# Optimization experiments

Hardware: AMD Instinct MI355X
Metric: run time of the kernel (lower is better)

The kernel has to match this reference:

```python
import jax, jax.numpy as jnp
import numpy as np

D_MODEL = 512
N_HEADS = 4  # d_model >= 8 -> 4 heads
HEAD_DIM = D_MODEL // N_HEADS
D_FF = 4 * D_MODEL


def setup_inputs() -> dict:
    key = jax.random.key(0)
    ks = jax.random.split(key, 8)
    B, T = 4, 2048
    s = 0.02
    return {
        "x": jax.random.normal(ks[0], (B, T, D_MODEL), dtype=jnp.float32),
        "ln1_g": jnp.ones((D_MODEL,), jnp.float32),
        "ln1_b": jnp.zeros((D_MODEL,), jnp.float32),
        "w_qkv": jax.random.normal(ks[1], (D_MODEL, 3 * D_MODEL), jnp.float32) * s,
        "w_proj": jax.random.normal(ks[2], (D_MODEL, D_MODEL), jnp.float32) * s,
        "ln2_g": jnp.ones((D_MODEL,), jnp.float32),
        "ln2_b": jnp.zeros((D_MODEL,), jnp.float32),
        "w_ff1": jax.random.normal(ks[3], (D_MODEL, D_FF), jnp.float32) * s,
        "w_ff2": jax.random.normal(ks[4], (D_FF, D_MODEL), jnp.float32) * s,
    }


def _layernorm(x, g, b, eps=1e-5):
    mu = jnp.mean(x, axis=-1, keepdims=True)
    var = jnp.var(x, axis=-1, keepdims=True)
    return (x - mu) * jax.lax.rsqrt(var + eps) * g + b


def _attention(x, w_qkv, w_proj):
    B, T, C = x.shape
    qkv = x @ w_qkv  # [B,T,3C]
    q, k, v = jnp.split(qkv, 3, axis=-1)
    # [B,H,T,Dh]
    q = q.reshape(B, T, N_HEADS, HEAD_DIM).transpose(0, 2, 1, 3)
    k = k.reshape(B, T, N_HEADS, HEAD_DIM).transpose(0, 2, 1, 3)
    v = v.reshape(B, T, N_HEADS, HEAD_DIM).transpose(0, 2, 1, 3)
    scale = 1.0 / jnp.sqrt(jnp.asarray(HEAD_DIM, x.dtype))
    scores = jnp.einsum("bhqd,bhkd->bhqk", q, k) * scale
    causal = jnp.tril(jnp.ones((T, T), bool))
    scores = jnp.where(causal, scores, -jnp.inf)
    attn = jax.nn.softmax(scores, axis=-1)
    out = jnp.einsum("bhqk,bhkd->bhqd", attn, v)
    out = out.transpose(0, 2, 1, 3).reshape(B, T, C)
    return out @ w_proj


def reference(x, ln1_g, ln1_b, w_qkv, w_proj, ln2_g, ln2_b, w_ff1, w_ff2):
    x = x + _attention(_layernorm(x, ln1_g, ln1_b), w_qkv, w_proj)
    h = _layernorm(x, ln2_g, ln2_b)
    h = jax.nn.gelu(h @ w_ff1, approximate=False) @ w_ff2
    return x + h
```

## Files before the change

### kernel.cpp

```cpp
#include <hip/hip_runtime.h>
#include <cstdint>

typedef unsigned short u16;
typedef __attribute__((ext_vector_type(8))) short short8;
typedef __attribute__((ext_vector_type(4))) float floatx4;

#define BT    8192
#define TSEQ  2048
#define NBAT  4
#define CMOD  512
#define NH    4
#define HD    128
#define DFF   2048
#define CQKV  1536

__device__ __forceinline__ u16 f2bf(float f) {
  union { float f; uint32_t u; } v; v.f = f;
  uint32_t r = v.u + 0x7FFFu + ((v.u >> 16) & 1u);
  return (u16)(r >> 16);
}
__device__ __forceinline__ float bf2f(u16 u) {
  union { uint32_t u; float f; } v; v.u = ((uint32_t)u) << 16; return v.f;
}
__device__ __forceinline__ float exp2a(float x) {
  float r; asm("v_exp_f32 %0, %1" : "=v"(r) : "v"(x)); return r;
}
__device__ __forceinline__ float rcpa(float x) {
  float r; asm("v_rcp_f32 %0, %1" : "=v"(r) : "v"(x)); return r;
}

typedef __attribute__((address_space(1))) const unsigned int ga_u32;
typedef __attribute__((address_space(3))) unsigned int ls_u32;
__device__ __forceinline__ void glds16(const u16* g, u16* l) {
  __builtin_amdgcn_global_load_lds((ga_u32*)g, (ls_u32*)l, 16, 0, 0);
}

__device__ __forceinline__ void tcast_body(const float* __restrict__ W, u16* __restrict__ Wt,
                                           int K, int N, int bx, int by, int tid,
                                           float (*tile)[33]) {
  int n0 = bx * 32, k0 = by * 32;
  int tx = tid & 31, ty = tid >> 5;
  #pragma unroll
  for (int r = 0; r < 32; r += 8)
    tile[r + ty][tx] = W[(size_t)(k0 + r + ty) * N + n0 + tx];
  __syncthreads();
  #pragma unroll
  for (int r = 0; r < 32; r += 8)
    Wt[(size_t)(n0 + r + ty) * K + k0 + tx] = f2bf(tile[tx][r + ty]);
}

__global__ __launch_bounds__(256) void prep_kernel(
    const float* __restrict__ x, const float* __restrict__ g, const float* __restrict__ b,
    const float* __restrict__ wqkv, const float* __restrict__ wproj,
    const float* __restrict__ wff1, const float* __restrict__ wff2,
    u16* __restrict__ ln_out, u16* __restrict__ wqkvT, u16* __restrict__ wprojT,
    u16* __restrict__ wff1T, u16* __restrict__ wff2T) {
  __shared__ float tile[32][33];
  int bid = blockIdx.x, tid = threadIdx.x;
  if (bid < 768) {
    tcast_body(wqkv, wqkvT, CMOD, CQKV, bid % 48, bid / 48, tid, tile);
  } else if (bid < 1024) {
    int id = bid - 768; tcast_body(wproj, wprojT, CMOD, CMOD, id % 16, id / 16, tid, tile);
  } else if (bid < 2048) {
    int id = bid - 1024; tcast_body(wff1, wff1T, CMOD, DFF, id % 64, id / 64, tid, tile);
  } else if (bid < 3072) {
    int id = bid - 2048; tcast_body(wff2, wff2T, DFF, CMOD, id % 16, id / 16, tid, tile);
  } else {
    int row = (bid - 3072) * 4 + (tid >> 6);
    int lane = tid & 63;
    const float4* xr = (const float4*)(x + (size_t)row * CMOD);
    float4 a = xr[lane], c = xr[lane + 64];
    float s = a.x + a.y + a.z + a.w + c.x + c.y + c.z + c.w;
    float q = a.x*a.x + a.y*a.y + a.z*a.z + a.w*a.w
            + c.x*c.x + c.y*c.y + c.z*c.z + c.w*c.w;
    #pragma unroll
    for (int o = 32; o; o >>= 1) { s += __shfl_xor(s, o); q += __shfl_xor(q, o); }
    float mu = s * (1.0f / CMOD);
    float rstd = rsqrtf(q * (1.0f / CMOD) - mu * mu + 1e-5f);
    const float4* gr = (const float4*)g;
    const float4* br = (const float4*)b;
    float4 g0 = gr[lane], g1 = gr[lane + 64], b0 = br[lane], b1 = br[lane + 64];
    u16* orow = ln_out + (size_t)row * CMOD;
    int i0 = lane * 4, i1 = (lane + 64) * 4;
    orow[i0 + 0] = f2bf((a.x - mu) * rstd * g0.x + b0.x);
    orow[i0 + 1] = f2bf((a.y - mu) * rstd * g0.y + b0.y);
    orow[i0 + 2] = f2bf((a.z - mu) * rstd * g0.z + b0.z);
    orow[i0 + 3] = f2bf((a.w - mu) * rstd * g0.w + b0.w);
    orow[i1 + 0] = f2bf((c.x - mu) * rstd * g1.x + b1.x);
    orow[i1 + 1] = f2bf((c.y - mu) * rstd * g1.y + b1.y);
    orow[i1 + 2] = f2bf((c.z - mu) * rstd * g1.z + b1.z);
    orow[i1 + 3] = f2bf((c.w - mu) * rstd * g1.w + b1.w);
  }
}

__global__ __launch_bounds__(256) void ln_kernel(const float* __restrict__ x,
                                                 const float* __restrict__ g,
                                                 const float* __restrict__ b,
                                                 u16* __restrict__ out) {
  int row = blockIdx.x * 4 + (threadIdx.x >> 6);
  int lane = threadIdx.x & 63;
  const float4* xr = (const float4*)(x + (size_t)row * CMOD);
  float4 a = xr[lane], c = xr[lane + 64];
  float s = a.x + a.y + a.z + a.w + c.x + c.y + c.z + c.w;
  float q = a.x*a.x + a.y*a.y + a.z*a.z + a.w*a.w
          + c.x*c.x + c.y*c.y + c.z*c.z + c.w*c.w;
  #pragma unroll
  for (int o = 32; o; o >>= 1) { s += __shfl_xor(s, o); q += __shfl_xor(q, o); }
  float mu = s * (1.0f / CMOD);
  float rstd = rsqrtf(q * (1.0f / CMOD) - mu * mu + 1e-5f);
  const float4* gr = (const float4*)g;
  const float4* br = (const float4*)b;
  float4 g0 = gr[lane], g1 = gr[lane + 64], b0 = br[lane], b1 = br[lane + 64];
  u16* orow = out + (size_t)row * CMOD;
  int i0 = lane * 4, i1 = (lane + 64) * 4;
  orow[i0 + 0] = f2bf((a.x - mu) * rstd * g0.x + b0.x);
  orow[i0 + 1] = f2bf((a.y - mu) * rstd * g0.y + b0.y);
  orow[i0 + 2] = f2bf((a.z - mu) * rstd * g0.z + b0.z);
  orow[i0 + 3] = f2bf((a.w - mu) * rstd * g0.w + b0.w);
  orow[i1 + 0] = f2bf((c.x - mu) * rstd * g1.x + b1.x);
  orow[i1 + 1] = f2bf((c.y - mu) * rstd * g1.y + b1.y);
  orow[i1 + 2] = f2bf((c.z - mu) * rstd * g1.z + b1.z);
  orow[i1 + 3] = f2bf((c.w - mu) * rstd * g1.w + b1.w);
}

template <int EPI, int TM, int TN, int MINW>
__global__ __launch_bounds__(256, MINW) void gemm_kernel(
    const u16* __restrict__ A, const u16* __restrict__ Bt, int K,
    const float* __restrict__ resid, float* __restrict__ outf,
    u16* __restrict__ ob0, u16* __restrict__ ob1, u16* __restrict__ ob2) {
  constexpr int MR  = TM / 32;
  constexpr int NR  = TN / 32;
  constexpr int NAR = TM / 64;
  constexpr int NBR = TN / 64;
  __shared__ __align__(16) u16 As[2][TM * 32];
  __shared__ __align__(16) u16 Bs[2][TN * 32];
  int tid = threadIdx.x;
  int lane = tid & 63, wave = tid >> 6;
  int lane16 = lane & 15, quad = lane >> 4;
  int n1d = blockIdx.x;
  int m0 = (n1d & 63) * TM;
  int n0 = (n1d >> 6) * TN;
  int wm = (wave >> 1) * (TM / 2), wn = (wave & 1) * (TN / 2);

  floatx4 acc[MR][NR];
  #pragma unroll
  for (int i = 0; i < MR; i++)
    #pragma unroll
    for (int j = 0; j < NR; j++) acc[i][j] = (floatx4)(0.0f);

  const u16* agp[NAR]; u16* alp[NAR][2];
  const u16* bgp[NBR]; u16* blp[NBR][2];
  #pragma unroll
  for (int i = 0; i < NAR; i++) {
    int s = i * 256 + tid;
    agp[i] = A + (size_t)(m0 + (s >> 2)) * K + (s & 3) * 8;
    alp[i][0] = &As[0][(i * 256 + wave * 64) * 8];
    alp[i][1] = &As[1][(i * 256 + wave * 64) * 8];
  }
  #pragma unroll
  for (int i = 0; i < NBR; i++) {
    int s = i * 256 + tid;
    bgp[i] = Bt + (size_t)(n0 + (s >> 2)) * K + (s & 3) * 8;
    blp[i][0] = &Bs[0][(i * 256 + wave * 64) * 8];
    blp[i][1] = &Bs[1][(i * 256 + wave * 64) * 8];
  }

  int nk = K >> 5;
  #pragma unroll
  for (int i = 0; i < NAR; i++) glds16(agp[i], alp[i][0]);
  #pragma unroll
  for (int i = 0; i < NBR; i++) glds16(bgp[i], blp[i][0]);

  for (int kt = 0; kt < nk; kt++) {
    __syncthreads();
    int buf = kt & 1;
    if (kt + 1 < nk) {
      int k1 = (kt + 1) * 32;
      #pragma unroll
      for (int i = 0; i < NAR; i++) glds16(agp[i] + k1, alp[i][buf ^ 1]);
      #pragma unroll
      for (int i = 0; i < NBR; i++) glds16(bgp[i] + k1, blp[i][buf ^ 1]);
    }
    short8 af[MR];
    #pragma unroll
    for (int i = 0; i < MR; i++)
      af[i] = *(const short8*)&As[buf][(wm + i * 16 + lane16) * 32 + quad * 8];
    #pragma unroll
    for (int j = 0; j < NR; j++) {
      short8 bfj = *(const short8*)&Bs[buf][(wn + j * 16 + lane16) * 32 + quad * 8];
      #pragma unroll
      for (int i = 0; i < MR; i++)
        acc[i][j] = __builtin_amdgcn_mfma_f32_16x16x32_bf16(af[i], bfj, acc[i][j], 0, 0, 0);
    }
  }

  #pragma unroll
  for (int i = 0; i < MR; i++) {
    #pragma unroll
    for (int j = 0; j < NR; j++) {
      #pragma unroll
      for (int r = 0; r < 4; r++) {
        int m = m0 + wm + i * 16 + quad * 4 + r;
        int n = n0 + wn + j * 16 + lane16;
        float v = acc[i][j][r];
        if (EPI == 0) {
          int bb = m >> 11, t = m & 2047;
          int nn = n & 511, which = n >> 9;
          int h = nn >> 7, d = nn & 127;
          size_t base = (size_t)(bb * NH + h) * 262144;
          if (which == 0) {
            int t16 = t >> 4, l16 = t & 15, cc = d >> 5, qd = (d >> 3) & 3, e = d & 7;
            ob0[base + (size_t)((t16 * 16 + cc * 4 + qd) * 128 + l16 * 8 + e)] = f2bf(v * 0.12751743f);
          } else if (which == 1) {
            int kt = t >> 5, hf = (t >> 4) & 1, l16 = t & 15, cc = d >> 5, qd = (d >> 3) & 3, e = d & 7;
            ob1[base + (size_t)((kt * 8 + hf * 4 + cc) * 512 + qd * 128 + l16 * 8 + e)] = f2bf(v);
          } else {
            int kt = t >> 5, qv = (t >> 3) & 3, e = t & 7, j2 = d >> 4, l16 = d & 15;
            ob2[base + (size_t)((kt * 8 + j2) * 512 + qv * 128 + l16 * 8 + e)] = f2bf(v);
          }
        } else if (EPI == 1) {
          size_t idx = (size_t)m * CMOD + n;
          outf[idx] = v + resid[idx];
        } else if (EPI == 2) {
          float ge = 0.5f * v * (1.0f + erff(v * 0.70710678118654752f));
          ob0[(size_t)m * DFF + n] = f2bf(ge);
        } else {
          size_t idx = (size_t)m * CMOD + n;
          outf[idx] = v + resid[idx];
        }
      }
    }
  }
}

__global__ __launch_bounds__(128) void attn_kernel(const u16* __restrict__ qb,
                                                   const u16* __restrict__ kb,
                                                   const u16* __restrict__ vtb,
                                                   u16* __restrict__ po,
                                                   float* __restrict__ pl) {
  int tid = threadIdx.x, wave = tid >> 6, lane = tid & 63;
  int lane16 = lane & 15, quad = lane >> 4;
  int n1d = blockIdx.x;
  int bh = n1d & 15;
  int idx = 143 - (n1d >> 4);
  int g = 1;
  #pragma unroll
  for (int t = 2; t <= 8; t++) if (idx >= 2 * t * (t - 1)) g = t;
  int rem = idx - 2 * g * (g - 1);
  int qi = rem / g;
  int c  = rem - qi * g;
  int qt = ((g - 1) << 2) + qi;

  int q0w = qt * 64 + wave * 32;
  const u16* Qb = qb  + (size_t)bh * 262144;
  const u16* Kb = kb  + (size_t)bh * 262144;
  const u16* Vb = vtb + (size_t)bh * 262144;

  short8 aqA[4], aqB[4];
  {
    int t16 = q0w >> 4;
    #pragma unroll
    for (int cc = 0; cc < 4; cc++) {
      aqA[cc] = *(const short8*)&Qb[(size_t)((t16 * 16 + cc * 4 + quad) * 128 + lane16 * 8)];
      aqB[cc] = *(const short8*)&Qb[(size_t)(((t16 + 1) * 16 + cc * 4 + quad) * 128 + lane16 * 8)];
    }
  }

  int ktw   = (q0w >> 5) + 1;
  int ktblk = qt * 2 + 2;
  int kt0   = c * 8;
  int kend  = min(min(kt0 + 8, ktblk), ktw);

  floatx4 oA[8], oB[8];
  #pragma unroll
  for (int j = 0; j < 8; j++) { oA[j] = (floatx4)(0.0f); oB[j] = (floatx4)(0.0f); }
  floatx4 olA = (floatx4)(0.0f), olB = (floatx4)(0.0f);

  short8 ones;
  #pragma unroll
  for (int e = 0; e < 8; e++) ones[e] = (short)0x3F80;

  int addrA = (lane16 + ((quad & 1) << 5)) << 2;
  int addrB = addrA + 64;
  int q_gA = q0w + lane16;
  int q_gB = q0w + 16 + lane16;

#define ATTN_TAIL(S0, S1, O_, OL_, QG, KT)                                                          \
  {                                                                                                 \
    int k0b = (KT) * 32 + quad * 4;                                                                 \
    _Pragma("unroll")                                                                               \
    for (int r = 0; r < 4; r++) {                                                                   \
      float p0 = exp2a(S0[r]);                                                                      \
      float p1 = exp2a(S1[r]);                                                                      \
      if (k0b + r > (QG)) p0 = 0.0f;                                                                \
      if (k0b + r + 16 > (QG)) p1 = 0.0f;                                                           \
      S0[r] = p0; S1[r] = p1;                                                                       \
    }                                                                                               \
    uint32_t x0 = __builtin_amdgcn_perm(__float_as_uint(S0[1]), __float_as_uint(S0[0]), 0x07060302u); \
    uint32_t x1 = __builtin_amdgcn_perm(__float_as_uint(S0[3]), __float_as_uint(S0[2]), 0x07060302u); \
    uint32_t y0 = __builtin_amdgcn_perm(__float_as_uint(S1[1]), __float_as_uint(S1[0]), 0x07060302u); \
    uint32_t y1 = __builtin_amdgcn_perm(__float_as_uint(S1[3]), __float_as_uint(S1[2]), 0x07060302u); \
    int pAx0 = __builtin_amdgcn_ds_bpermute(addrA, (int)x0);                                        \
    int pAx1 = __builtin_amdgcn_ds_bpermute(addrA, (int)x1);                                        \
    int pBx0 = __builtin_amdgcn_ds_bpermute(addrB, (int)x0);                                        \
    int pBx1 = __builtin_amdgcn_ds_bpermute(addrB, (int)x1);                                        \
    int pAy0 = __builtin_amdgcn_ds_bpermute(addrA, (int)y0);                                        \
    int pAy1 = __builtin_amdgcn_ds_bpermute(addrA, (int)y1);                                        \
    int pBy0 = __builtin_amdgcn_ds_bpermute(addrB, (int)y0);                                        \
    int pBy1 = __builtin_amdgcn_ds_bpermute(addrB, (int)y1);                                        \
    union { uint32_t u[4]; short8 s; } pf;                                                          \
    bool hi = quad >= 2;                                                                            \
    pf.u[0] = (uint32_t)(hi ? pAy0 : pAx0);                                                         \
    pf.u[1] = (uint32_t)(hi ? pAy1 : pAx1);                                                         \
    pf.u[2] = (uint32_t)(hi ? pBy0 : pBx0);                                                         \
    pf.u[3] = (uint32_t)(hi ? pBy1 : pBx1);                                                         \
    _Pragma("unroll")                                                                               \
    for (int j = 0; j < 8; j++)                                                                     \
      O_[j] = __builtin_amdgcn_mfma_f32_16x16x32_bf16(pf.s, vfr[j], O_[j], 0, 0, 0);                \
    OL_ = __builtin_amdgcn_mfma_f32_16x16x32_bf16(pf.s, ones, OL_, 0, 0, 0);                        \
  }

  for (int kt = kt0; kt < kend; kt++) {
    const u16* kp = Kb + (size_t)kt * 4096 + lane * 8;
    const u16* vp = Vb + (size_t)kt * 4096 + lane * 8;
    short8 k0f[4], k1f[4];
    #pragma unroll
    for (int cc = 0; cc < 4; cc++) {
      k0f[cc] = *(const short8*)&kp[cc * 512];
      k1f[cc] = *(const short8*)&kp[(4 + cc) * 512];
    }

    floatx4 sA0 = (floatx4)(0.0f), sA1 = (floatx4)(0.0f);
    floatx4 sB0 = (floatx4)(0.0f), sB1 = (floatx4)(0.0f);
    #pragma unroll
    for (int cc = 0; cc < 4; cc++) {
      sA0 = __builtin_amdgcn_mfma_f32_16x16x32_bf16(k0f[cc], aqA[cc], sA0, 0, 0, 0);
      sA1 = __builtin_amdgcn_mfma_f32_16x16x32_bf16(k1f[cc], aqA[cc], sA1, 0, 0, 0);
      sB0 = __builtin_amdgcn_mfma_f32_16x16x32_bf16(k0f[cc], aqB[cc], sB0, 0, 0, 0);
      sB1 = __builtin_amdgcn_mfma_f32_16x16x32_bf16(k1f[cc], aqB[cc], sB1, 0, 0, 0);
    }

    short8 vfr[8];
    #pragma unroll
    for (int j = 0; j < 8; j++)
      vfr[j] = *(const short8*)&vp[j * 512];

    ATTN_TAIL(sA0, sA1, oA, olA, q_gA, kt);
    ATTN_TAIL(sB0, sB1, oB, olB, q_gB, kt);
  }
#undef ATTN_TAIL

  int slot = bh * 144 + 2 * g * (g - 1) + qi * g + c;
  u16* pob = po + (size_t)slot * 8192;
  #pragma unroll
  for (int r = 0; r < 4; r++) {
    int qrA = wave * 32 + quad * 4 + r;
    int qrB = qrA + 16;
    #pragma unroll
    for (int j = 0; j < 8; j++) {
      pob[qrA * 128 + j * 16 + lane16] = f2bf(oA[j][r]);
      pob[qrB * 128 + j * 16 + lane16] = f2bf(oB[j][r]);
    }
    if (lane16 == 0) {
      pl[slot * 64 + qrA] = olA[r];
      pl[slot * 64 + qrB] = olB[r];
    }
  }
}

__global__ __launch_bounds__(256) void reduce_kernel(const u16* __restrict__ po,
                                                     const float* __restrict__ pl,
                                                     u16* __restrict__ attn) {
  int bh = blockIdx.x >> 5, qt = blockIdx.x & 31;
  int tid = threadIdx.x;
  int g = (qt >> 2) + 1;
  int slot0 = bh * 144 + 2 * g * (g - 1) + (qt & 3) * g;
  int qrow = tid >> 2;
  int d0 = (tid & 3) * 32;
  float acc[32];
  #pragma unroll
  for (int i = 0; i < 32; i++) acc[i] = 0.0f;
  float l = 0.0f;
  for (int c = 0; c < g; c++) {
    int slot = slot0 + c;
    l += pl[slot * 64 + qrow];
    const short8* p = (const short8*)(po + (size_t)slot * 8192 + qrow * 128 + d0);
    #pragma unroll
    for (int v = 0; v < 4; v++) {
      short8 pk = p[v];
      #pragma unroll
      for (int e = 0; e < 8; e++) acc[v * 8 + e] += bf2f((u16)pk[e]);
    }
  }
  float inv = rcpa(l);
  int b = bh >> 2, h = bh & 3, t = qt * 64 + qrow;
  u16* orow = attn + ((size_t)(b * TSEQ + t)) * CMOD + h * HD + d0;
  #pragma unroll
  for (int v = 0; v < 4; v++) {
    short8 ov;
    #pragma unroll
    for (int e = 0; e < 8; e++) ov[e] = (short)f2bf(acc[v * 8 + e] * inv);
    *(short8*)(orow + v * 8) = ov;
  }
}

extern "C" void kernel_launch(void* const* d_in, const int* in_sizes, int n_in,
                              void* d_out, int out_size, void* d_ws, size_t ws_size,
                              hipStream_t stream) {
  const float* x     = (const float*)d_in[0];
  const float* ln1g  = (const float*)d_in[1];
  const float* ln1b  = (const float*)d_in[2];
  const float* wqkv  = (const float*)d_in[3];
  const float* wproj = (const float*)d_in[4];
  const float* ln2g  = (const float*)d_in[5];
  const float* ln2b  = (const float*)d_in[6];
  const float* wff1  = (const float*)d_in[7];
  const float* wff2  = (const float*)d_in[8];
  float* out = (float*)d_out;
  char* ws = (char*)d_ws;

  u16* wt_qkv  = (u16*)(ws);
  u16* wt_proj = (u16*)(ws + 1572864);
  u16* wt_ff1  = (u16*)(ws + 2097152);
  u16* wt_ff2  = (u16*)(ws + 4194304);
  u16* ln_buf  = (u16*)(ws + 6291456);
  u16* q_buf   = (u16*)(ws + 14680064);
  u16* k_buf   = (u16*)(ws + 23068672);
  u16* vt_buf  = (u16*)(ws + 31457280);
  u16* attn    = (u16*)(ws + 39845888);
  float* x2    = (float*)(ws + 48234496);
  u16* h1      = (u16*)(ws + 65011712);
  u16* po      = (u16*)(ws + 48234496);
  float* pl    = (float*)(ws + 85983232);

  dim3 blk(256);
  prep_kernel<<<dim3(5120), blk, 0, stream>>>(x, ln1g, ln1b, wqkv, wproj, wff1, wff2,
                                              ln_buf, wt_qkv, wt_proj, wt_ff1, wt_ff2);

  gemm_kernel<0, 128, 64, 6><<<dim3((CQKV / 64) * 64), blk, 0, stream>>>(
      ln_buf, wt_qkv, CMOD, nullptr, nullptr, q_buf, k_buf, vt_buf);

  attn_kernel<<<dim3(2304), dim3(128), 0, stream>>>(q_buf, k_buf, vt_buf, po, pl);

  reduce_kernel<<<dim3(512), blk, 0, stream>>>(po, pl, attn);

  gemm_kernel<1, 128, 64, 4><<<dim3((CMOD / 64) * 64), blk, 0, stream>>>(
      attn, wt_proj, CMOD, x, x2, nullptr, nullptr, nullptr);

  ln_kernel<<<dim3(BT / 4), blk, 0, stream>>>(x2, ln2g, ln2b, ln_buf);

  gemm_kernel<2, 128, 64, 6><<<dim3((DFF / 64) * 64), blk, 0, stream>>>(
      ln_buf, wt_ff1, CMOD, nullptr, nullptr, h1, nullptr, nullptr);

  gemm_kernel<3, 128, 64, 4><<<dim3((CMOD / 64) * 64), blk, 0, stream>>>(
      h1, wt_ff2, DFF, x2, out, nullptr, nullptr, nullptr);
}
```

Measured before the change: 250.4 us.

## Pre-swizzle LN output and weights into MFMA fragment layout for LDS-free GEMMs

```diff
diff --git a/kernel.cpp b/kernel.cpp
--- a/kernel.cpp
+++ b/kernel.cpp
@@ -35,9 +35,13 @@
   __builtin_amdgcn_global_load_lds((ga_u32*)g, (ls_u32*)l, 16, 0, 0);
 }
 
+__device__ __forceinline__ size_t af_idx(int row, int k, int nkt) {
+  return (size_t)((row >> 4) * nkt + (k >> 5)) * 512 + ((k >> 3) & 3) * 128 + (row & 15) * 8 + (k & 7);
+}
+
 __device__ __forceinline__ void tcast_body(const float* __restrict__ W, u16* __restrict__ Wt,
                                            int K, int N, int bx, int by, int tid,
-                                           float (*tile)[33]) {
+                                           float (*tile)[33], int BFMT) {
   int n0 = bx * 32, k0 = by * 32;
   int tx = tid & 31, ty = tid >> 5;
   #pragma unroll
@@ -45,8 +49,13 @@
     tile[r + ty][tx] = W[(size_t)(k0 + r + ty) * N + n0 + tx];
   __syncthreads();
   #pragma unroll
-  for (int r = 0; r < 32; r += 8)
-    Wt[(size_t)(n0 + r + ty) * K + k0 + tx] = f2bf(tile[tx][r + ty]);
+  for (int r = 0; r < 32; r += 8) {
+    int nr = n0 + r + ty, k = k0 + tx;
+    if (BFMT)
+      Wt[af_idx(nr, k, K >> 5)] = f2bf(tile[tx][r + ty]);
+    else
+      Wt[(size_t)nr * K + k] = f2bf(tile[tx][r + ty]);
+  }
 }
 
 __global__ __launch_bounds__(256) void prep_kernel(
@@ -58,13 +67,13 @@
   __shared__ float tile[32][33];
   int bid = blockIdx.x, tid = threadIdx.x;
   if (bid < 768) {
-    tcast_body(wqkv, wqkvT, CMOD, CQKV, bid % 48, bid / 48, tid, tile);
+    tcast_body(wqkv, wqkvT, CMOD, CQKV, bid % 48, bid / 48, tid, tile, 1);
   } else if (bid < 1024) {
-    int id = bid - 768; tcast_body(wproj, wprojT, CMOD, CMOD, id % 16, id / 16, tid, tile);
+    int id = bid - 768; tcast_body(wproj, wprojT, CMOD, CMOD, id % 16, id / 16, tid, tile, 0);
   } else if (bid < 2048) {
-    int id = bid - 1024; tcast_body(wff1, wff1T, CMOD, DFF, id % 64, id / 64, tid, tile);
+    int id = bid - 1024; tcast_body(wff1, wff1T, CMOD, DFF, id % 64, id / 64, tid, tile, 1);
   } else if (bid < 3072) {
-    int id = bid - 2048; tcast_body(wff2, wff2T, DFF, CMOD, id % 16, id / 16, tid, tile);
+    int id = bid - 2048; tcast_body(wff2, wff2T, DFF, CMOD, id % 16, id / 16, tid, tile, 0);
   } else {
     int row = (bid - 3072) * 4 + (tid >> 6);
     int lane = tid & 63;
@@ -80,16 +89,17 @@
     const float4* gr = (const float4*)g;
     const float4* br = (const float4*)b;
     float4 g0 = gr[lane], g1 = gr[lane + 64], b0 = br[lane], b1 = br[lane + 64];
-    u16* orow = ln_out + (size_t)row * CMOD;
-    int i0 = lane * 4, i1 = (lane + 64) * 4;
-    orow[i0 + 0] = f2bf((a.x - mu) * rstd * g0.x + b0.x);
-    orow[i0 + 1] = f2bf((a.y - mu) * rstd * g0.y + b0.y);
-    orow[i0 + 2] = f2bf((a.z - mu) * rstd * g0.z + b0.z);
-    orow[i0 + 3] = f2bf((a.w - mu) * rstd * g0.w + b0.w);
-    orow[i1 + 0] = f2bf((c.x - mu) * rstd * g1.x + b1.x);
-    orow[i1 + 1] = f2bf((c.y - mu) * rstd * g1.y + b1.y);
-    orow[i1 + 2] = f2bf((c.z - mu) * rstd * g1.z + b1.z);
-    orow[i1 + 3] = f2bf((c.w - mu) * rstd * g1.w + b1.w);
+    int c0 = lane * 4, c1 = (lane + 64) * 4;
+    u16* o0 = ln_out + af_idx(row, c0, 16);
+    u16* o1 = ln_out + af_idx(row, c1, 16);
+    o0[0] = f2bf((a.x - mu) * rstd * g0.x + b0.x);
+    o0[1] = f2bf((a.y - mu) * rstd * g0.y + b0.y);
+    o0[2] = f2bf((a.z - mu) * rstd * g0.z + b0.z);
+    o0[3] = f2bf((a.w - mu) * rstd * g0.w + b0.w);
+    o1[0] = f2bf((c.x - mu) * rstd * g1.x + b1.x);
+    o1[1] = f2bf((c.y - mu) * rstd * g1.y + b1.y);
+    o1[2] = f2bf((c.z - mu) * rstd * g1.z + b1.z);
+    o1[3] = f2bf((c.w - mu) * rstd * g1.w + b1.w);
   }
 }
 
@@ -111,23 +121,90 @@
   const float4* gr = (const float4*)g;
   const float4* br = (const float4*)b;
   float4 g0 = gr[lane], g1 = gr[lane + 64], b0 = br[lane], b1 = br[lane + 64];
-  u16* orow = out + (size_t)row * CMOD;
-  int i0 = lane * 4, i1 = (lane + 64) * 4;
-  orow[i0 + 0] = f2bf((a.x - mu) * rstd * g0.x + b0.x);
-  orow[i0 + 1] = f2bf((a.y - mu) * rstd * g0.y + b0.y);
-  orow[i0 + 2] = f2bf((a.z - mu) * rstd * g0.z + b0.z);
-  orow[i0 + 3] = f2bf((a.w - mu) * rstd * g0.w + b0.w);
-  orow[i1 + 0] = f2bf((c.x - mu) * rstd * g1.x + b1.x);
-  orow[i1 + 1] = f2bf((c.y - mu) * rstd * g1.y + b1.y);
-  orow[i1 + 2] = f2bf((c.z - mu) * rstd * g1.z + b1.z);
-  orow[i1 + 3] = f2bf((c.w - mu) * rstd * g1.w + b1.w);
+  int c0 = lane * 4, c1 = (lane + 64) * 4;
+  u16* o0 = out + af_idx(row, c0, 16);
+  u16* o1 = out + af_idx(row, c1, 16);
+  o0[0] = f2bf((a.x - mu) * rstd * g0.x + b0.x);
+  o0[1] = f2bf((a.y - mu) * rstd * g0.y + b0.y);
+  o0[2] = f2bf((a.z - mu) * rstd * g0.z + b0.z);
+  o0[3] = f2bf((a.w - mu) * rstd * g0.w + b0.w);
+  o1[0] = f2bf((c.x - mu) * rstd * g1.x + b1.x);
+  o1[1] = f2bf((c.y - mu) * rstd * g1.y + b1.y);
+  o1[2] = f2bf((c.z - mu) * rstd * g1.z + b1.z);
+  o1[3] = f2bf((c.w - mu) * rstd * g1.w + b1.w);
+}
+
+template <int EPI>
+__global__ __launch_bounds__(256) void gemm_frag(
+    const u16* __restrict__ AF, const u16* __restrict__ BF,
+    u16* __restrict__ ob0, u16* __restrict__ ob1, u16* __restrict__ ob2) {
+  int tid = threadIdx.x;
+  int lane = tid & 63, wave = tid >> 6;
+  int lane16 = lane & 15, quad = lane >> 4;
+  int mb = blockIdx.x & 63, nb = blockIdx.x >> 6;
+  int mw = mb * 128 + (wave >> 1) * 64;
+  int nw = nb * 128 + (wave & 1) * 64;
+  const u16* ap = AF + (size_t)mw * 512 + lane * 8;
+  const u16* bp = BF + (size_t)nw * 512 + lane * 8;
+
+  floatx4 acc[4][4];
+  #pragma unroll
+  for (int i = 0; i < 4; i++)
+    #pragma unroll
+    for (int j = 0; j < 4; j++) acc[i][j] = (floatx4)(0.0f);
+
+  for (int kt = 0; kt < 16; kt++) {
+    short8 af[4], bf[4];
+    #pragma unroll
+    for (int i = 0; i < 4; i++)
+      af[i] = *(const short8*)(ap + (size_t)(i * 16 + kt) * 512);
+    #pragma unroll
+    for (int j = 0; j < 4; j++)
+      bf[j] = *(const short8*)(bp + (size_t)(j * 16 + kt) * 512);
+    #pragma unroll
+    for (int j = 0; j < 4; j++)
+      #pragma unroll
+      for (int i = 0; i < 4; i++)
+        acc[i][j] = __builtin_amdgcn_mfma_f32_16x16x32_bf16(af[i], bf[j], acc[i][j], 0, 0, 0);
+  }
+
+  #pragma unroll
+  for (int i = 0; i < 4; i++) {
+    #pragma unroll
+    for (int j = 0; j < 4; j++) {
+      #pragma unroll
+      for (int r = 0; r < 4; r++) {
+        int m = mw + i * 16 + quad * 4 + r;
+        int n = nw + j * 16 + lane16;
+        float v = acc[i][j][r];
+        if (EPI == 0) {
+          int bb = m >> 11, t = m & 2047;
+          int nn = n & 511, which = n >> 9;
+          int h = nn >> 7, d = nn & 127;
+          size_t base = (size_t)(bb * NH + h) * 262144;
+          if (which == 0) {
+            int t16 = t >> 4, l16 = t & 15, cc = d >> 5, qd = (d >> 3) & 3, e = d & 7;
+            ob0[base + (size_t)((t16 * 16 + cc * 4 + qd) * 128 + l16 * 8 + e)] = f2bf(v * 0.12751743f);
+          } else if (which == 1) {
+            int kt2 = t >> 5, hf = (t >> 4) & 1, l16 = t & 15, cc = d >> 5, qd = (d >> 3) & 3, e = d & 7;
+            ob1[base + (size_t)((kt2 * 8 + hf * 4 + cc) * 512 + qd * 128 + l16 * 8 + e)] = f2bf(v);
+          } else {
+            int kt2 = t >> 5, qv = (t >> 3) & 3, e = t & 7, j2 = d >> 4, l16 = d & 15;
+            ob2[base + (size_t)((kt2 * 8 + j2) * 512 + qv * 128 + l16 * 8 + e)] = f2bf(v);
+          }
+        } else {
+          float ge = 0.5f * v * (1.0f + erff(v * 0.70710678118654752f));
+          ob0[(size_t)m * DFF + n] = f2bf(ge);
+        }
+      }
+    }
+  }
 }
 
 template <int EPI, int TM, int TN, int MINW>
 __global__ __launch_bounds__(256, MINW) void gemm_kernel(
     const u16* __restrict__ A, const u16* __restrict__ Bt, int K,
-    const float* __restrict__ resid, float* __restrict__ outf,
-    u16* __restrict__ ob0, u16* __restrict__ ob1, u16* __restrict__ ob2) {
+    const float* __restrict__ resid, float* __restrict__ outf) {
   constexpr int MR  = TM / 32;
   constexpr int NR  = TN / 32;
   constexpr int NAR = TM / 64;
@@ -203,31 +280,8 @@
         int m = m0 + wm + i * 16 + quad * 4 + r;
         int n = n0 + wn + j * 16 + lane16;
         float v = acc[i][j][r];
-        if (EPI == 0) {
-          int bb = m >> 11, t = m & 2047;
-          int nn = n & 511, which = n >> 9;
-          int h = nn >> 7, d = nn & 127;
-          size_t base = (size_t)(bb * NH + h) * 262144;
-          if (which == 0) {
-            int t16 = t >> 4, l16 = t & 15, cc = d >> 5, qd = (d >> 3) & 3, e = d & 7;
-            ob0[base + (size_t)((t16 * 16 + cc * 4 + qd) * 128 + l16 * 8 + e)] = f2bf(v * 0.12751743f);
-          } else if (which == 1) {
-            int kt = t >> 5, hf = (t >> 4) & 1, l16 = t & 15, cc = d >> 5, qd = (d >> 3) & 3, e = d & 7;
-            ob1[base + (size_t)((kt * 8 + hf * 4 + cc) * 512 + qd * 128 + l16 * 8 + e)] = f2bf(v);
-          } else {
-            int kt = t >> 5, qv = (t >> 3) & 3, e = t & 7, j2 = d >> 4, l16 = d & 15;
-            ob2[base + (size_t)((kt * 8 + j2) * 512 + qv * 128 + l16 * 8 + e)] = f2bf(v);
-          }
-        } else if (EPI == 1) {
-          size_t idx = (size_t)m * CMOD + n;
-          outf[idx] = v + resid[idx];
-        } else if (EPI == 2) {
-          float ge = 0.5f * v * (1.0f + erff(v * 0.70710678118654752f));
-          ob0[(size_t)m * DFF + n] = f2bf(ge);
-        } else {
-          size_t idx = (size_t)m * CMOD + n;
-          outf[idx] = v + resid[idx];
-        }
+        size_t idx = (size_t)m * CMOD + n;
+        outf[idx] = v + resid[idx];
       }
     }
   }
@@ -437,21 +491,19 @@
   prep_kernel<<<dim3(5120), blk, 0, stream>>>(x, ln1g, ln1b, wqkv, wproj, wff1, wff2,
                                               ln_buf, wt_qkv, wt_proj, wt_ff1, wt_ff2);
 
-  gemm_kernel<0, 128, 64, 6><<<dim3((CQKV / 64) * 64), blk, 0, stream>>>(
-      ln_buf, wt_qkv, CMOD, nullptr, nullptr, q_buf, k_buf, vt_buf);
+  gemm_frag<0><<<dim3(768), blk, 0, stream>>>(ln_buf, wt_qkv, q_buf, k_buf, vt_buf);
 
   attn_kernel<<<dim3(2304), dim3(128), 0, stream>>>(q_buf, k_buf, vt_buf, po, pl);
 
   reduce_kernel<<<dim3(512), blk, 0, stream>>>(po, pl, attn);
 
   gemm_kernel<1, 128, 64, 4><<<dim3((CMOD / 64) * 64), blk, 0, stream>>>(
-      attn, wt_proj, CMOD, x, x2, nullptr, nullptr, nullptr);
+      attn, wt_proj, CMOD, x, x2);
 
   ln_kernel<<<dim3(BT / 4), blk, 0, stream>>>(x2, ln2g, ln2b, ln_buf);
 
-  gemm_kernel<2, 128, 64, 6><<<dim3((DFF / 64) * 64), blk, 0, stream>>>(
-      ln_buf, wt_ff1, CMOD, nullptr, nullptr, h1, nullptr, nullptr);
+  gemm_frag<2><<<dim3(1024), blk, 0, stream>>>(ln_buf, wt_ff1, h1, nullptr, nullptr);
 
   gemm_kernel<3, 128, 64, 4><<<dim3((CMOD / 64) * 64), blk, 0, stream>>>(
-      h1, wt_ff2, DFF, x2, out, nullptr, nullptr, nullptr);
-}
+      h1, wt_ff2, DFF, x2, out);
+}
```

After: 254.4 us. About the same (+1.6%).
